# Performance work log

Hardware: AMD Instinct MI355X
Metric: run time of the kernel (lower is better)

## Reference

```python
import jax, jax.numpy as jnp
import numpy as np

NEG = -1e20
EPS = float(np.finfo(np.float32).eps)


def setup_inputs() -> dict:
    key = jax.random.key(0)
    k1, k2, k3, k4 = jax.random.split(key, 4)
    B, S, E, D = 8, 2048, 1024, 1024
    return {
        "embeddings": jax.random.normal(k1, (B, S, E), dtype=jnp.float32),
        "mask": jnp.ones((B, S), dtype=jnp.int32),
        "W_q": jax.random.normal(k2, (E, D), dtype=jnp.float32),
        "W_k": jax.random.normal(k3, (E, D), dtype=jnp.float32),
        "W_v": jax.random.normal(k4, (E, D), dtype=jnp.float32),
    }


def reference(embeddings, mask, W_q, W_k, W_v):
    # embeddings: [B,S,E]; mask: [B,S] (1 = keep, 0 = pad)
    q = embeddings @ W_q            # [B,S,D]
    k = embeddings @ W_k            # [B,S,D]
    v = embeddings @ W_v            # [B,S,Dv]
    energy = jnp.einsum("bqd,bkd->bqk", q, k)  # [B,S,S]
    S = embeddings.shape[1]
    causal = jnp.tril(jnp.ones((S, S), dtype=bool))          # [S,S]
    energy = jnp.where(causal[None, :, :], energy, NEG)
    pad = (mask == 0)[:, None, :]                             # [B,1,S]
    energy = jnp.where(pad, NEG, energy)
    d_k = jnp.float32(W_k.shape[1])
    scale = jnp.sqrt(d_k) + EPS
    attention = jax.nn.softmax(energy / scale, axis=-1)       # [B,S,S]
    output = jnp.einsum("bqk,bkd->bqd", attention, v)         # [B,S,Dv]
    return output, attention
```

## Files before the change

kernel.cpp:

```cpp
#include <hip/hip_runtime.h>

#define Bb 8
#define Ss 2048
#define Ee 1024
#define Dd 1024

typedef __attribute__((ext_vector_type(8))) __bf16 bf16x8;
typedef __attribute__((ext_vector_type(4))) float f32x4;
typedef unsigned short u16;

__device__ __forceinline__ u16 f2bf(float x) {
  unsigned u = __float_as_uint(x);
  return (u16)((u + 0x7fffu + ((u >> 16) & 1u)) >> 16);
}
__device__ __forceinline__ float bf2f(u16 h) {
  return __uint_as_float(((unsigned)h) << 16);
}

__device__ __forceinline__ void gload16(const void* g, void* l) {
  __builtin_amdgcn_global_load_lds(
      (__attribute__((address_space(1))) void*)const_cast<void*>(g),
      (__attribute__((address_space(3))) void*)l, 16, 0, 0);
}

#define MFMA_BF16 __builtin_amdgcn_mfma_f32_16x16x32_bf16

__global__ __launch_bounds__(256) void k_split4(const float* __restrict__ in,
                                                u16* __restrict__ hi,
                                                u16* __restrict__ lo,
                                                long long n4) {
  long long i = (long long)blockIdx.x * 256 + threadIdx.x;
  if (i >= n4) return;
  float4 v = ((const float4*)in)[i];
  float xs[4] = {v.x, v.y, v.z, v.w};
  u16 hh[4], ll[4];
#pragma unroll
  for (int j = 0; j < 4; ++j) {
    hh[j] = f2bf(xs[j]);
    ll[j] = f2bf(xs[j] - bf2f(hh[j]));
  }
  ushort4 h, l;
  h.x = hh[0]; h.y = hh[1]; h.z = hh[2]; h.w = hh[3];
  l.x = ll[0]; l.y = ll[1]; l.z = ll[2]; l.w = ll[3];
  ((ushort4*)hi)[i] = h;
  ((ushort4*)lo)[i] = l;
}

__global__ __launch_bounds__(256) void k_wt_split(const float* __restrict__ W,
                                                  u16* __restrict__ hi,
                                                  u16* __restrict__ lo) {
  __shared__ float t[32][33];
  const int tx = threadIdx.x & 31;
  const int ty = threadIdx.x >> 5;
  const int e0 = blockIdx.y * 32, d0 = blockIdx.x * 32;
#pragma unroll
  for (int r = ty; r < 32; r += 8)
    t[r][tx] = W[(long long)(e0 + r) * Dd + d0 + tx];
  __syncthreads();
#pragma unroll
  for (int r = ty; r < 32; r += 8) {
    float x = t[tx][r];
    long long o = (long long)(d0 + r) * Ee + e0 + tx;
    u16 h = f2bf(x);
    hi[o] = h;
    if (lo) lo[o] = f2bf(x - bf2f(h));
  }
}

template <int NP, int EPI, bool CAUSAL, bool TRIK>
__global__ __launch_bounds__(512, 4) void k_t128(
    const u16* __restrict__ Ah, const u16* __restrict__ Al,
    const u16* __restrict__ Bh, const u16* __restrict__ Bl,
    float* __restrict__ Cf, u16* __restrict__ Ch, u16* __restrict__ Cl,
    int nbx, int N, int K, long long strA, long long strB, long long strC) {
  constexpr int NMAT = (NP == 3) ? 4 : 2;
  const int nwg = gridDim.x;
  const int f = blockIdx.x;
  const int wgid = (f & 7) * (nwg >> 3) + (f >> 3);
  int bx, by, bz;
  if (CAUSAL) {
    bz = wgid / 136;
    const int t = wgid % 136;
    int yy = 0, c = 0;
    while (c + yy + 1 <= t) { c += yy + 1; ++yy; }
    by = yy;
    bx = t - c;
  } else {
    bz = blockIdx.y;
    bx = wgid % nbx;
    by = wgid / nbx;
  }

  __shared__ __align__(16) u16 lds[2][NMAT][4096];

  const int tid = threadIdx.x;
  const int lane = tid & 63;
  const int w = tid >> 6;
  const int wr = w >> 1;
  const int wc = w & 1;

  const u16* srcBase[NMAT];
  if constexpr (NP == 3) {
    srcBase[0] = Ah + (long long)bz * strA;
    srcBase[1] = Al + (long long)bz * strA;
    srcBase[2] = Bh + (long long)bz * strB;
    srcBase[3] = Bl + (long long)bz * strB;
  } else {
    srcBase[0] = Ah + (long long)bz * strA;
    srcBase[1] = Bh + (long long)bz * strB;
  }
  const long long row0[2] = {(long long)by * 128, (long long)bx * 128};

  const int rL = tid >> 2;
  const int colOff = ((tid & 3) ^ ((tid >> 3) & 3)) * 8;
  const int rdOff = (lane & 15) * 64 + ((((lane >> 4) & 3) ^ ((lane >> 1) & 3)) << 4);

  const int AR = wr * 32;
  const int BR = wc * 64;
  int nt = K / 32;
  if (TRIK) {
    const int lim = ((by + 1) * 128) / 32;
    if (lim < nt) nt = lim;
  }

  const u16* gp[NMAT];
#pragma unroll
  for (int m = 0; m < NMAT; ++m) {
    const int opsel = (NP == 3) ? (m >> 1) : m;
    gp[m] = srcBase[m] + (row0[opsel] + rL) * (long long)K + colOff;
  }

#define STG(BUF)                                                       \
  {                                                                    \
    _Pragma("unroll") for (int m = 0; m < NMAT; ++m) {                 \
      gload16(gp[m], (char*)&lds[BUF][m][0] + tid * 16);               \
      gp[m] += 32;                                                     \
    }                                                                  \
  }
#define LDFRAG(MAT, R) \
  (*(const bf16x8*)((const char*)&lds[cur][MAT][0] + (R)*64 + rdOff))
#define BAR __builtin_amdgcn_s_barrier()

#define CLUSTER3(NH)                                                         \
  __builtin_amdgcn_s_setprio(1);                                             \
  _Pragma("unroll") for (int m = 0; m < 2; ++m)                              \
      _Pragma("unroll") for (int n = 0; n < 2; ++n)                          \
          acc[m][(NH)*2 + n] =                                               \
      MFMA_BF16(aH[m], bL[n], acc[m][(NH)*2 + n], 0, 0, 0);                  \
  _Pragma("unroll") for (int m = 0; m < 2; ++m)                              \
      _Pragma("unroll") for (int n = 0; n < 2; ++n)                          \
          acc[m][(NH)*2 + n] =                                               \
      MFMA_BF16(aL[m], bH[n], acc[m][(NH)*2 + n], 0, 0, 0);                  \
  _Pragma("unroll") for (int m = 0; m < 2; ++m)                              \
      _Pragma("unroll") for (int n = 0; n < 2; ++n)                          \
          acc[m][(NH)*2 + n] =                                               \
      MFMA_BF16(aH[m], bH[n], acc[m][(NH)*2 + n], 0, 0, 0);                  \
  __builtin_amdgcn_s_setprio(0);

  f32x4 acc[2][4];
#pragma unroll
  for (int m = 0; m < 2; ++m)
#pragma unroll
    for (int n = 0; n < 4; ++n) acc[m][n] = f32x4{0.f, 0.f, 0.f, 0.f};

  bf16x8 aH[2], aL[2], bH[2], bL[2];
  bf16x8 bF[4];

  STG(0);

  for (int kt = 0; kt < nt; ++kt) {
    const int cur = kt & 1;
    const bool more = (kt + 1 < nt);

    if (more) {
      STG(cur ^ 1);
      if constexpr (NP == 3)
        asm volatile("s_waitcnt vmcnt(4)" ::: "memory");
      else
        asm volatile("s_waitcnt vmcnt(2)" ::: "memory");
    } else {
      asm volatile("s_waitcnt vmcnt(0)" ::: "memory");
    }
    BAR;

    if constexpr (NP == 3) {
#pragma unroll
      for (int m = 0; m < 2; ++m) {
        aH[m] = LDFRAG(0, AR + m * 16);
        aL[m] = LDFRAG(1, AR + m * 16);
      }
#pragma unroll
      for (int n = 0; n < 2; ++n) {
        bH[n] = LDFRAG(2, BR + n * 16);
        bL[n] = LDFRAG(3, BR + n * 16);
      }
      BAR;
      CLUSTER3(0);
      BAR;
#pragma unroll
      for (int n = 0; n < 2; ++n) {
        bH[n] = LDFRAG(2, BR + 32 + n * 16);
        bL[n] = LDFRAG(3, BR + 32 + n * 16);
      }
      BAR;
      CLUSTER3(1);
      BAR;
    } else {
#pragma unroll
      for (int m = 0; m < 2; ++m) aH[m] = LDFRAG(0, AR + m * 16);
#pragma unroll
      for (int n = 0; n < 4; ++n) bF[n] = LDFRAG(1, BR + n * 16);
      BAR;
      __builtin_amdgcn_s_setprio(1);
#pragma unroll
      for (int m = 0; m < 2; ++m)
#pragma unroll
        for (int n = 0; n < 4; ++n)
          acc[m][n] = MFMA_BF16(aH[m], bF[n], acc[m][n], 0, 0, 0);
      __builtin_amdgcn_s_setprio(0);
      BAR;
    }
  }

  const int cr = (lane >> 4) << 2;
  const int cc = lane & 15;
#pragma unroll
  for (int m = 0; m < 2; ++m)
#pragma unroll
    for (int n = 0; n < 4; ++n)
#pragma unroll
      for (int r = 0; r < 4; ++r) {
        const long long row = (long long)by * 128 + wr * 32 + m * 16 + cr + r;
        const long long col = (long long)bx * 128 + wc * 64 + n * 16 + cc;
        const float v = acc[m][n][r];
        if constexpr (EPI == 0) {
          Cf[(long long)bz * strC + row * N + col] = v;
        } else if constexpr (EPI == 1) {
          const long long idx = row * N + col;
          u16 h = f2bf(v);
          Ch[idx] = h;
          Cl[idx] = f2bf(v - bf2f(h));
        } else {
          Ch[(long long)bz * strC + row * N + col] = f2bf(v);
        }
      }
#undef STG
#undef LDFRAG
#undef BAR
#undef CLUSTER3
}

__global__ __launch_bounds__(256) void k_softmax(float* __restrict__ attn,
                                                 u16* __restrict__ attn_bf,
                                                 const int* __restrict__ mask,
                                                 float inv_scale) {
  const int q = blockIdx.x;
  const int b = blockIdx.y;
  const int tid = threadIdx.x;
  float* row = attn + ((long long)b * Ss + q) * Ss;
  u16* rowb = attn_bf + ((long long)b * Ss + q) * Ss;
  const int* mrow = mask + b * Ss;
  const int qup = ((q >> 7) + 1) << 7;

  float x[8];
  float m = -3.0e38f;
#pragma unroll
  for (int j = 0; j < 8; ++j) {
    const int k = tid + j * 256;
    float v = -3.0e38f;
    if (k <= q) {
      const float e = row[k];
      v = ((mrow[k] != 0) ? e : -1e20f) * inv_scale;
    }
    x[j] = v;
    m = fmaxf(m, v);
  }
#pragma unroll
  for (int o = 32; o > 0; o >>= 1) m = fmaxf(m, __shfl_xor(m, o));
  __shared__ float redm[4], reds[4];
  const int w = tid >> 6;
  if ((tid & 63) == 0) redm[w] = m;
  __syncthreads();
  m = fmaxf(fmaxf(redm[0], redm[1]), fmaxf(redm[2], redm[3]));
  float s = 0.f;
#pragma unroll
  for (int j = 0; j < 8; ++j) {
    x[j] = __expf(x[j] - m);
    s += x[j];
  }
#pragma unroll
  for (int o = 32; o > 0; o >>= 1) s += __shfl_xor(s, o);
  if ((tid & 63) == 0) reds[w] = s;
  __syncthreads();
  s = reds[0] + reds[1] + reds[2] + reds[3];
  const float inv = 1.0f / s;
#pragma unroll
  for (int j = 0; j < 8; ++j) {
    const int k = tid + j * 256;
    if (k <= q) {
      const float a = x[j] * inv;
      row[k] = a;
      rowb[k] = f2bf(a);
    } else {
      row[k] = 0.0f;
      if (k < qup) rowb[k] = 0;
    }
  }
}

extern "C" void kernel_launch(void* const* d_in, const int* in_sizes, int n_in,
                              void* d_out, int out_size, void* d_ws, size_t ws_size,
                              hipStream_t stream) {
  const float* emb = (const float*)d_in[0];
  const int* mask = (const int*)d_in[1];
  const float* Wq = (const float*)d_in[2];
  const float* Wk = (const float*)d_in[3];
  const float* Wv = (const float*)d_in[4];

  float* out = (float*)d_out;
  float* attn = out + (long long)Bb * Ss * Dd;

  char* p = (char*)d_ws;
  u16* emb_hi = (u16*)p;
  u16* emb_lo = emb_hi + 16777216LL;
  u16* R_hi = (u16*)(p + 67108864LL);
  u16* R_lo = R_hi + 16777216LL;
  u16* v_t = R_lo + 16777216LL;
  u16* attn_bf = v_t + 16777216LL;
  u16* Wqr_hi = attn_bf + 16777216LL;
  u16* Wqr_lo = Wqr_hi + 1048576LL;
  u16* Wkr_hi = Wqr_lo + 1048576LL;
  u16* Wkr_lo = Wkr_hi + 1048576LL;
  u16* M_hi = Wkr_lo + 1048576LL;
  u16* M_lo = M_hi + 1048576LL;
  u16* WvT_hi = M_lo + 1048576LL;

  const float inv_scale = 1.0f / (32.0f + 1.1920929e-07f);

  k_split4<<<16384, 256, 0, stream>>>(emb, emb_hi, emb_lo, 4194304LL);
  k_split4<<<1024, 256, 0, stream>>>(Wq, Wqr_hi, Wqr_lo, 262144LL);
  k_split4<<<1024, 256, 0, stream>>>(Wk, Wkr_hi, Wkr_lo, 262144LL);
  k_wt_split<<<dim3(32, 32), 256, 0, stream>>>(Wv, WvT_hi, nullptr);

  k_t128<3, 1, false, false><<<64, 512, 0, stream>>>(
      Wkr_hi, Wkr_lo, Wqr_hi, Wqr_lo, nullptr, M_hi, M_lo,
      8, 1024, 1024, 0, 0, 0);
  k_t128<3, 1, false, false><<<1024, 512, 0, stream>>>(
      emb_hi, emb_lo, M_hi, M_lo, nullptr, R_hi, R_lo,
      8, 1024, 1024, 0, 0, 0);
  k_t128<1, 2, false, false><<<dim3(128, 8), 512, 0, stream>>>(
      WvT_hi, nullptr, emb_hi, nullptr, nullptr, v_t, nullptr,
      16, Ss, Ee, 0, (long long)Ss * Ee, (long long)Dd * Ss);
  k_t128<3, 0, true, false><<<1088, 512, 0, stream>>>(
      R_hi, R_lo, emb_hi, emb_lo, attn, nullptr, nullptr,
      0, Ss, Dd, (long long)Ss * Dd, (long long)Ss * Dd, (long long)Ss * Ss);
  k_softmax<<<dim3(Ss, Bb), 256, 0, stream>>>(attn, attn_bf, mask, inv_scale);
  k_t128<1, 0, false, true><<<dim3(128, 8), 512, 0, stream>>>(
      attn_bf, nullptr, v_t, nullptr, out, nullptr, nullptr,
      8, Dd, Ss, (long long)Ss * Ss, (long long)Dd * Ss, (long long)Ss * Dd);
}
```

Baseline: 469.6 us.

## Enlarge GEMM tiles to 256x128 with 64x64 per-warp output blocks

Changes the shared GEMM kernel from 128x128 to 256x128 workgroup tiles, so each warp now computes a 64x64 block (4x4 MFMA fragments) instead of 32x64. This raises operand reuse from LDS and drops the extra mid-iteration barriers and split fragment loads. The causal tile enumeration, the softmax padding boundary and all grid sizes are updated to match. In exchange it uses more LDS and registers per workgroup (min occupancy lowered to 2 for the 3-pass path) and launches fewer workgroups, which may hurt load balance.

```diff
diff --git a/kernel.cpp b/kernel.cpp
--- a/kernel.cpp
+++ b/kernel.cpp
@@ -68,21 +68,27 @@
 }
 
 template <int NP, int EPI, bool CAUSAL, bool TRIK>
-__global__ __launch_bounds__(512, 4) void k_t128(
+__global__ __launch_bounds__(512, (NP == 3) ? 2 : 4) void k_t256(
     const u16* __restrict__ Ah, const u16* __restrict__ Al,
     const u16* __restrict__ Bh, const u16* __restrict__ Bl,
     float* __restrict__ Cf, u16* __restrict__ Ch, u16* __restrict__ Cl,
     int nbx, int N, int K, long long strA, long long strB, long long strC) {
-  constexpr int NMAT = (NP == 3) ? 4 : 2;
+  constexpr int NLD = (NP == 3) ? 6 : 3;
+  constexpr int LDSB = (NP == 3) ? 49152 : 24576;
+  constexpr int OFF_AL = 16384;
+  constexpr int OFF_BH = (NP == 3) ? 32768 : 16384;
+  constexpr int OFF_BL = 40960;
+  __shared__ __align__(16) char lds[2][LDSB];
+
   const int nwg = gridDim.x;
   const int f = blockIdx.x;
   const int wgid = (f & 7) * (nwg >> 3) + (f >> 3);
   int bx, by, bz;
   if (CAUSAL) {
-    bz = wgid / 136;
-    const int t = wgid % 136;
+    bz = wgid / 72;
+    const int t = wgid % 72;
     int yy = 0, c = 0;
-    while (c + yy + 1 <= t) { c += yy + 1; ++yy; }
+    while (c + 2 * yy + 2 <= t) { c += 2 * yy + 2; ++yy; }
     by = yy;
     bx = t - c;
   } else {
@@ -91,80 +97,62 @@
     by = wgid / nbx;
   }
 
-  __shared__ __align__(16) u16 lds[2][NMAT][4096];
-
   const int tid = threadIdx.x;
   const int lane = tid & 63;
   const int w = tid >> 6;
   const int wr = w >> 1;
   const int wc = w & 1;
-
-  const u16* srcBase[NMAT];
-  if constexpr (NP == 3) {
-    srcBase[0] = Ah + (long long)bz * strA;
-    srcBase[1] = Al + (long long)bz * strA;
-    srcBase[2] = Bh + (long long)bz * strB;
-    srcBase[3] = Bl + (long long)bz * strB;
-  } else {
-    srcBase[0] = Ah + (long long)bz * strA;
-    srcBase[1] = Bh + (long long)bz * strB;
-  }
-  const long long row0[2] = {(long long)by * 128, (long long)bx * 128};
+  const int AR = wr * 64;
+  const int BR = wc * 64;
 
   const int rL = tid >> 2;
   const int colOff = ((tid & 3) ^ ((tid >> 3) & 3)) * 8;
   const int rdOff = (lane & 15) * 64 + ((((lane >> 4) & 3) ^ ((lane >> 1) & 3)) << 4);
 
-  const int AR = wr * 32;
-  const int BR = wc * 64;
+  const long long rowA0 = (long long)by * 256;
+  const long long rowB0 = (long long)bx * 128;
+
   int nt = K / 32;
   if (TRIK) {
-    const int lim = ((by + 1) * 128) / 32;
+    const int lim = (by + 1) * 8;
     if (lim < nt) nt = lim;
   }
 
-  const u16* gp[NMAT];
-#pragma unroll
-  for (int m = 0; m < NMAT; ++m) {
-    const int opsel = (NP == 3) ? (m >> 1) : m;
-    gp[m] = srcBase[m] + (row0[opsel] + rL) * (long long)K + colOff;
-  }
-
-#define STG(BUF)                                                       \
-  {                                                                    \
-    _Pragma("unroll") for (int m = 0; m < NMAT; ++m) {                 \
-      gload16(gp[m], (char*)&lds[BUF][m][0] + tid * 16);               \
-      gp[m] += 32;                                                     \
-    }                                                                  \
-  }
-#define LDFRAG(MAT, R) \
-  (*(const bf16x8*)((const char*)&lds[cur][MAT][0] + (R)*64 + rdOff))
+  const u16* gp[NLD];
+  int dst[NLD];
+  if constexpr (NP == 3) {
+    const u16* pAh = Ah + (long long)bz * strA;
+    const u16* pAl = Al + (long long)bz * strA;
+    const u16* pBh = Bh + (long long)bz * strB;
+    const u16* pBl = Bl + (long long)bz * strB;
+    gp[0] = pAh + (rowA0 + rL) * (long long)K + colOff;       dst[0] = tid * 16;
+    gp[1] = pAh + (rowA0 + 128 + rL) * (long long)K + colOff; dst[1] = 8192 + tid * 16;
+    gp[2] = pAl + (rowA0 + rL) * (long long)K + colOff;       dst[2] = OFF_AL + tid * 16;
+    gp[3] = pAl + (rowA0 + 128 + rL) * (long long)K + colOff; dst[3] = OFF_AL + 8192 + tid * 16;
+    gp[4] = pBh + (rowB0 + rL) * (long long)K + colOff;       dst[4] = OFF_BH + tid * 16;
+    gp[5] = pBl + (rowB0 + rL) * (long long)K + colOff;       dst[5] = OFF_BL + tid * 16;
+  } else {
+    const u16* pA = Ah + (long long)bz * strA;
+    const u16* pB = Bh + (long long)bz * strB;
+    gp[0] = pA + (rowA0 + rL) * (long long)K + colOff;        dst[0] = tid * 16;
+    gp[1] = pA + (rowA0 + 128 + rL) * (long long)K + colOff;  dst[1] = 8192 + tid * 16;
+    gp[2] = pB + (rowB0 + rL) * (long long)K + colOff;        dst[2] = OFF_BH + tid * 16;
+  }
+
+#define STG(BUF)                                               \
+  {                                                            \
+    _Pragma("unroll") for (int u = 0; u < NLD; ++u) {          \
+      gload16(gp[u], lds[BUF] + dst[u]);                       \
+      gp[u] += 32;                                             \
+    }                                                          \
+  }
 #define BAR __builtin_amdgcn_s_barrier()
 
-#define CLUSTER3(NH)                                                         \
-  __builtin_amdgcn_s_setprio(1);                                             \
-  _Pragma("unroll") for (int m = 0; m < 2; ++m)                              \
-      _Pragma("unroll") for (int n = 0; n < 2; ++n)                          \
-          acc[m][(NH)*2 + n] =                                               \
-      MFMA_BF16(aH[m], bL[n], acc[m][(NH)*2 + n], 0, 0, 0);                  \
-  _Pragma("unroll") for (int m = 0; m < 2; ++m)                              \
-      _Pragma("unroll") for (int n = 0; n < 2; ++n)                          \
-          acc[m][(NH)*2 + n] =                                               \
-      MFMA_BF16(aL[m], bH[n], acc[m][(NH)*2 + n], 0, 0, 0);                  \
-  _Pragma("unroll") for (int m = 0; m < 2; ++m)                              \
-      _Pragma("unroll") for (int n = 0; n < 2; ++n)                          \
-          acc[m][(NH)*2 + n] =                                               \
-      MFMA_BF16(aH[m], bH[n], acc[m][(NH)*2 + n], 0, 0, 0);                  \
-  __builtin_amdgcn_s_setprio(0);
-
-  f32x4 acc[2][4];
-#pragma unroll
-  for (int m = 0; m < 2; ++m)
+  f32x4 acc[4][4];
+#pragma unroll
+  for (int m = 0; m < 4; ++m)
 #pragma unroll
     for (int n = 0; n < 4; ++n) acc[m][n] = f32x4{0.f, 0.f, 0.f, 0.f};
-
-  bf16x8 aH[2], aL[2], bH[2], bL[2];
-  bf16x8 bF[4];
 
   STG(0);
 
@@ -175,63 +163,69 @@
     if (more) {
       STG(cur ^ 1);
       if constexpr (NP == 3)
-        asm volatile("s_waitcnt vmcnt(4)" ::: "memory");
+        asm volatile("s_waitcnt vmcnt(6)" ::: "memory");
       else
-        asm volatile("s_waitcnt vmcnt(2)" ::: "memory");
+        asm volatile("s_waitcnt vmcnt(3)" ::: "memory");
     } else {
       asm volatile("s_waitcnt vmcnt(0)" ::: "memory");
     }
     BAR;
 
+    const char* bb = lds[cur];
     if constexpr (NP == 3) {
-#pragma unroll
-      for (int m = 0; m < 2; ++m) {
-        aH[m] = LDFRAG(0, AR + m * 16);
-        aL[m] = LDFRAG(1, AR + m * 16);
+      bf16x8 aH[4], aL[4], bH[4], bL[4];
+#pragma unroll
+      for (int m = 0; m < 4; ++m) {
+        aH[m] = *(const bf16x8*)(bb + (AR + m * 16) * 64 + rdOff);
+        aL[m] = *(const bf16x8*)(bb + OFF_AL + (AR + m * 16) * 64 + rdOff);
       }
 #pragma unroll
-      for (int n = 0; n < 2; ++n) {
-        bH[n] = LDFRAG(2, BR + n * 16);
-        bL[n] = LDFRAG(3, BR + n * 16);
+      for (int n = 0; n < 4; ++n) {
+        bH[n] = *(const bf16x8*)(bb + OFF_BH + (BR + n * 16) * 64 + rdOff);
+        bL[n] = *(const bf16x8*)(bb + OFF_BL + (BR + n * 16) * 64 + rdOff);
       }
-      BAR;
-      CLUSTER3(0);
-      BAR;
-#pragma unroll
-      for (int n = 0; n < 2; ++n) {
-        bH[n] = LDFRAG(2, BR + 32 + n * 16);
-        bL[n] = LDFRAG(3, BR + 32 + n * 16);
-      }
-      BAR;
-      CLUSTER3(1);
-      BAR;
+#pragma unroll
+      for (int m = 0; m < 4; ++m)
+#pragma unroll
+        for (int n = 0; n < 4; ++n)
+          acc[m][n] = MFMA_BF16(aH[m], bL[n], acc[m][n], 0, 0, 0);
+#pragma unroll
+      for (int m = 0; m < 4; ++m)
+#pragma unroll
+        for (int n = 0; n < 4; ++n)
+          acc[m][n] = MFMA_BF16(aL[m], bH[n], acc[m][n], 0, 0, 0);
+#pragma unroll
+      for (int m = 0; m < 4; ++m)
+#pragma unroll
+        for (int n = 0; n < 4; ++n)
+          acc[m][n] = MFMA_BF16(aH[m], bH[n], acc[m][n], 0, 0, 0);
     } else {
-#pragma unroll
-      for (int m = 0; m < 2; ++m) aH[m] = LDFRAG(0, AR + m * 16);
-#pragma unroll
-      for (int n = 0; n < 4; ++n) bF[n] = LDFRAG(1, BR + n * 16);
-      BAR;
-      __builtin_amdgcn_s_setprio(1);
-#pragma unroll
-      for (int m = 0; m < 2; ++m)
+      bf16x8 a[4], b[4];
+#pragma unroll
+      for (int m = 0; m < 4; ++m)
+        a[m] = *(const bf16x8*)(bb + (AR + m * 16) * 64 + rdOff);
+#pragma unroll
+      for (int n = 0; n < 4; ++n)
+        b[n] = *(const bf16x8*)(bb + OFF_BH + (BR + n * 16) * 64 + rdOff);
+#pragma unroll
+      for (int m = 0; m < 4; ++m)
 #pragma unroll
         for (int n = 0; n < 4; ++n)
-          acc[m][n] = MFMA_BF16(aH[m], bF[n], acc[m][n], 0, 0, 0);
-      __builtin_amdgcn_s_setprio(0);
-      BAR;
+          acc[m][n] = MFMA_BF16(a[m], b[n], acc[m][n], 0, 0, 0);
     }
+    BAR;
   }
 
   const int cr = (lane >> 4) << 2;
   const int cc = lane & 15;
 #pragma unroll
-  for (int m = 0; m < 2; ++m)
+  for (int m = 0; m < 4; ++m)
 #pragma unroll
     for (int n = 0; n < 4; ++n)
 #pragma unroll
       for (int r = 0; r < 4; ++r) {
-        const long long row = (long long)by * 128 + wr * 32 + m * 16 + cr + r;
-        const long long col = (long long)bx * 128 + wc * 64 + n * 16 + cc;
+        const long long row = (long long)by * 256 + AR + m * 16 + cr + r;
+        const long long col = (long long)bx * 128 + BR + n * 16 + cc;
         const float v = acc[m][n][r];
         if constexpr (EPI == 0) {
           Cf[(long long)bz * strC + row * N + col] = v;
@@ -245,9 +239,7 @@
         }
       }
 #undef STG
-#undef LDFRAG
 #undef BAR
-#undef CLUSTER3
 }
 
 __global__ __launch_bounds__(256) void k_softmax(float* __restrict__ attn,
@@ -260,7 +252,7 @@
   float* row = attn + ((long long)b * Ss + q) * Ss;
   u16* rowb = attn_bf + ((long long)b * Ss + q) * Ss;
   const int* mrow = mask + b * Ss;
-  const int qup = ((q >> 7) + 1) << 7;
+  const int qup = ((q >> 8) + 1) << 8;
 
   float x[8];
   float m = -3.0e38f;
@@ -342,20 +334,20 @@
   k_split4<<<1024, 256, 0, stream>>>(Wk, Wkr_hi, Wkr_lo, 262144LL);
   k_wt_split<<<dim3(32, 32), 256, 0, stream>>>(Wv, WvT_hi, nullptr);
 
-  k_t128<3, 1, false, false><<<64, 512, 0, stream>>>(
+  k_t256<3, 1, false, false><<<32, 512, 0, stream>>>(
       Wkr_hi, Wkr_lo, Wqr_hi, Wqr_lo, nullptr, M_hi, M_lo,
       8, 1024, 1024, 0, 0, 0);
-  k_t128<3, 1, false, false><<<1024, 512, 0, stream>>>(
+  k_t256<3, 1, false, false><<<512, 512, 0, stream>>>(
       emb_hi, emb_lo, M_hi, M_lo, nullptr, R_hi, R_lo,
       8, 1024, 1024, 0, 0, 0);
-  k_t128<1, 2, false, false><<<dim3(128, 8), 512, 0, stream>>>(
+  k_t256<1, 2, false, false><<<dim3(64, 8), 512, 0, stream>>>(
       WvT_hi, nullptr, emb_hi, nullptr, nullptr, v_t, nullptr,
       16, Ss, Ee, 0, (long long)Ss * Ee, (long long)Dd * Ss);
-  k_t128<3, 0, true, false><<<1088, 512, 0, stream>>>(
+  k_t256<3, 0, true, false><<<576, 512, 0, stream>>>(
       R_hi, R_lo, emb_hi, emb_lo, attn, nullptr, nullptr,
-      0, Ss, Dd, (long long)Ss * Dd, (long long)Ss * Dd, (long long)Ss * Ss);
+      0, Ss, Dd, (long long)Ss * Dd, (long long)Ss * Ee, (long long)Ss * Ss);
   k_softmax<<<dim3(Ss, Bb), 256, 0, stream>>>(attn, attn_bf, mask, inv_scale);
-  k_t128<1, 0, false, true><<<dim3(128, 8), 512, 0, stream>>>(
+  k_t256<1, 0, false, true><<<dim3(64, 8), 512, 0, stream>>>(
       attn_bf, nullptr, v_t, nullptr, out, nullptr, nullptr,
       8, Dd, Ss, (long long)Ss * Ss, (long long)Dd * Ss, (long long)Ss * Dd);
 }
```

Measured after the change: 468.7 us. Within noise of the previous version (-0.2%).

## Use 256x128 output tiles for projection, V and attention-times-V GEMMs

Applied to the files above, without the earlier changes.

Adds two new GEMM kernels with 256-row by 128-column tiles: a split-precision kernel (hi/lo bf16, three MFMA passes) for the emb·M projection, and a double-buffered single-precision-bf16 kernel for the V projection and the attention·V product. The larger tiles are meant to raise reuse of each B tile and halve the number of workgroups. The softmax zero-fill boundary is widened from 128 to 256 to match the triangular K limit of the new P·V tile. The split kernel has no double buffering, so load latency may be exposed, and the bigger tiles reduce parallelism for the smaller grids.

```diff
diff --git a/kernel.cpp b/kernel.cpp
--- a/kernel.cpp
+++ b/kernel.cpp
@@ -250,6 +250,218 @@
 #undef CLUSTER3
 }
 
+template <int EPI>
+__global__ __launch_bounds__(512, 4) void k_s256(
+    const u16* __restrict__ Ah, const u16* __restrict__ Al,
+    const u16* __restrict__ Bh, const u16* __restrict__ Bl,
+    float* __restrict__ Cf, u16* __restrict__ Ch, u16* __restrict__ Cl,
+    int nbx, int N, int K) {
+  constexpr int OFF_AL = 16384;
+  constexpr int OFF_BH = 32768;
+  constexpr int OFF_BL = 40960;
+  __shared__ __align__(16) char lds[49152];
+
+  const int nwg = gridDim.x;
+  const int f = blockIdx.x;
+  const int wgid = (f & 7) * (nwg >> 3) + (f >> 3);
+  const int bx = wgid % nbx;
+  const int by = wgid / nbx;
+
+  const int tid = threadIdx.x;
+  const int lane = tid & 63;
+  const int w = tid >> 6;
+  const int wr = w >> 1;
+  const int wc = w & 1;
+  const int AR = wr * 64;
+  const int BR = wc * 64;
+
+  const int rL = tid >> 2;
+  const int colOff = ((tid & 3) ^ ((tid >> 3) & 3)) * 8;
+  const int rdOff = (lane & 15) * 64 + ((((lane >> 4) & 3) ^ ((lane >> 1) & 3)) << 4);
+
+  const long long rowA0 = (long long)by * 256;
+  const long long rowB0 = (long long)bx * 128;
+  const int nt = K / 32;
+
+  const u16* gp[6];
+  int dst[6];
+  gp[0] = Ah + (rowA0 + rL) * (long long)K + colOff;        dst[0] = tid * 16;
+  gp[1] = Ah + (rowA0 + 128 + rL) * (long long)K + colOff;  dst[1] = 8192 + tid * 16;
+  gp[2] = Al + (rowA0 + rL) * (long long)K + colOff;        dst[2] = OFF_AL + tid * 16;
+  gp[3] = Al + (rowA0 + 128 + rL) * (long long)K + colOff;  dst[3] = OFF_AL + 8192 + tid * 16;
+  gp[4] = Bh + (rowB0 + rL) * (long long)K + colOff;        dst[4] = OFF_BH + tid * 16;
+  gp[5] = Bl + (rowB0 + rL) * (long long)K + colOff;        dst[5] = OFF_BL + tid * 16;
+
+  f32x4 acc[4][4];
+#pragma unroll
+  for (int m = 0; m < 4; ++m)
+#pragma unroll
+    for (int n = 0; n < 4; ++n) acc[m][n] = f32x4{0.f, 0.f, 0.f, 0.f};
+
+  for (int kt = 0; kt < nt; ++kt) {
+#pragma unroll
+    for (int u = 0; u < 6; ++u) {
+      gload16(gp[u], lds + dst[u]);
+      gp[u] += 32;
+    }
+    asm volatile("s_waitcnt vmcnt(0)" ::: "memory");
+    __builtin_amdgcn_s_barrier();
+
+    bf16x8 aH[4], aL[4];
+#pragma unroll
+    for (int m = 0; m < 4; ++m) {
+      aH[m] = *(const bf16x8*)(lds + (AR + m * 16) * 64 + rdOff);
+      aL[m] = *(const bf16x8*)(lds + OFF_AL + (AR + m * 16) * 64 + rdOff);
+    }
+#pragma unroll
+    for (int n = 0; n < 4; ++n) {
+      bf16x8 bH = *(const bf16x8*)(lds + OFF_BH + (BR + n * 16) * 64 + rdOff);
+      bf16x8 bL = *(const bf16x8*)(lds + OFF_BL + (BR + n * 16) * 64 + rdOff);
+#pragma unroll
+      for (int m = 0; m < 4; ++m)
+        acc[m][n] = MFMA_BF16(aH[m], bL, acc[m][n], 0, 0, 0);
+#pragma unroll
+      for (int m = 0; m < 4; ++m)
+        acc[m][n] = MFMA_BF16(aL[m], bH, acc[m][n], 0, 0, 0);
+#pragma unroll
+      for (int m = 0; m < 4; ++m)
+        acc[m][n] = MFMA_BF16(aH[m], bH, acc[m][n], 0, 0, 0);
+    }
+    __builtin_amdgcn_s_barrier();
+  }
+
+  const int cr = (lane >> 4) << 2;
+  const int cc = lane & 15;
+#pragma unroll
+  for (int m = 0; m < 4; ++m)
+#pragma unroll
+    for (int n = 0; n < 4; ++n)
+#pragma unroll
+      for (int r = 0; r < 4; ++r) {
+        const long long row = (long long)by * 256 + AR + m * 16 + cr + r;
+        const long long col = (long long)bx * 128 + BR + n * 16 + cc;
+        const float v = acc[m][n][r];
+        if constexpr (EPI == 0) {
+          Cf[row * N + col] = v;
+        } else {
+          const long long idx = row * N + col;
+          u16 h = f2bf(v);
+          Ch[idx] = h;
+          Cl[idx] = f2bf(v - bf2f(h));
+        }
+      }
+}
+
+template <int EPI, bool TRIK>
+__global__ __launch_bounds__(512, 4) void k_t256(
+    const u16* __restrict__ Ah, const u16* __restrict__ Bh,
+    float* __restrict__ Cf, u16* __restrict__ Ch,
+    int nbx, int N, int K, long long strA, long long strB, long long strC) {
+  constexpr int OFF_BH = 16384;
+  __shared__ __align__(16) char lds[2][24576];
+
+  const int nwg = gridDim.x;
+  const int f = blockIdx.x;
+  const int wgid = (f & 7) * (nwg >> 3) + (f >> 3);
+  const int bz = blockIdx.y;
+  const int bx = wgid % nbx;
+  const int by = wgid / nbx;
+
+  const int tid = threadIdx.x;
+  const int lane = tid & 63;
+  const int w = tid >> 6;
+  const int wr = w >> 1;
+  const int wc = w & 1;
+  const int AR = wr * 64;
+  const int BR = wc * 64;
+
+  const int rL = tid >> 2;
+  const int colOff = ((tid & 3) ^ ((tid >> 3) & 3)) * 8;
+  const int rdOff = (lane & 15) * 64 + ((((lane >> 4) & 3) ^ ((lane >> 1) & 3)) << 4);
+
+  const long long rowA0 = (long long)by * 256;
+  const long long rowB0 = (long long)bx * 128;
+
+  int nt = K / 32;
+  if (TRIK) {
+    const int lim = (by + 1) * 8;
+    if (lim < nt) nt = lim;
+  }
+
+  const u16* pA = Ah + (long long)bz * strA;
+  const u16* pB = Bh + (long long)bz * strB;
+  const u16* gp[3];
+  int dst[3];
+  gp[0] = pA + (rowA0 + rL) * (long long)K + colOff;        dst[0] = tid * 16;
+  gp[1] = pA + (rowA0 + 128 + rL) * (long long)K + colOff;  dst[1] = 8192 + tid * 16;
+  gp[2] = pB + (rowB0 + rL) * (long long)K + colOff;        dst[2] = OFF_BH + tid * 16;
+
+#define STG(BUF)                                               \
+  {                                                            \
+    _Pragma("unroll") for (int u = 0; u < 3; ++u) {            \
+      gload16(gp[u], lds[BUF] + dst[u]);                       \
+      gp[u] += 32;                                             \
+    }                                                          \
+  }
+#define BAR __builtin_amdgcn_s_barrier()
+
+  f32x4 acc[4][4];
+#pragma unroll
+  for (int m = 0; m < 4; ++m)
+#pragma unroll
+    for (int n = 0; n < 4; ++n) acc[m][n] = f32x4{0.f, 0.f, 0.f, 0.f};
+
+  STG(0);
+
+  for (int kt = 0; kt < nt; ++kt) {
+    const int cur = kt & 1;
+    const bool more = (kt + 1 < nt);
+
+    if (more) {
+      STG(cur ^ 1);
+      asm volatile("s_waitcnt vmcnt(3)" ::: "memory");
+    } else {
+      asm volatile("s_waitcnt vmcnt(0)" ::: "memory");
+    }
+    BAR;
+
+    const char* bb = lds[cur];
+    bf16x8 a[4], b[4];
+#pragma unroll
+    for (int m = 0; m < 4; ++m)
+      a[m] = *(const bf16x8*)(bb + (AR + m * 16) * 64 + rdOff);
+#pragma unroll
+    for (int n = 0; n < 4; ++n)
+      b[n] = *(const bf16x8*)(bb + OFF_BH + (BR + n * 16) * 64 + rdOff);
+#pragma unroll
+    for (int m = 0; m < 4; ++m)
+#pragma unroll
+      for (int n = 0; n < 4; ++n)
+        acc[m][n] = MFMA_BF16(a[m], b[n], acc[m][n], 0, 0, 0);
+    BAR;
+  }
+
+  const int cr = (lane >> 4) << 2;
+  const int cc = lane & 15;
+#pragma unroll
+  for (int m = 0; m < 4; ++m)
+#pragma unroll
+    for (int n = 0; n < 4; ++n)
+#pragma unroll
+      for (int r = 0; r < 4; ++r) {
+        const long long row = (long long)by * 256 + AR + m * 16 + cr + r;
+        const long long col = (long long)bx * 128 + BR + n * 16 + cc;
+        const float v = acc[m][n][r];
+        if constexpr (EPI == 0) {
+          Cf[(long long)bz * strC + row * N + col] = v;
+        } else {
+          Ch[(long long)bz * strC + row * N + col] = f2bf(v);
+        }
+      }
+#undef STG
+#undef BAR
+}
+
 __global__ __launch_bounds__(256) void k_softmax(float* __restrict__ attn,
                                                  u16* __restrict__ attn_bf,
                                                  const int* __restrict__ mask,
@@ -260,7 +472,7 @@
   float* row = attn + ((long long)b * Ss + q) * Ss;
   u16* rowb = attn_bf + ((long long)b * Ss + q) * Ss;
   const int* mrow = mask + b * Ss;
-  const int qup = ((q >> 7) + 1) << 7;
+  const int qup = ((q >> 8) + 1) << 8;
 
   float x[8];
   float m = -3.0e38f;
@@ -345,17 +557,16 @@
   k_t128<3, 1, false, false><<<64, 512, 0, stream>>>(
       Wkr_hi, Wkr_lo, Wqr_hi, Wqr_lo, nullptr, M_hi, M_lo,
       8, 1024, 1024, 0, 0, 0);
-  k_t128<3, 1, false, false><<<1024, 512, 0, stream>>>(
-      emb_hi, emb_lo, M_hi, M_lo, nullptr, R_hi, R_lo,
-      8, 1024, 1024, 0, 0, 0);
-  k_t128<1, 2, false, false><<<dim3(128, 8), 512, 0, stream>>>(
-      WvT_hi, nullptr, emb_hi, nullptr, nullptr, v_t, nullptr,
+  k_s256<1><<<512, 512, 0, stream>>>(
+      emb_hi, emb_lo, M_hi, M_lo, nullptr, R_hi, R_lo, 8, 1024, 1024);
+  k_t256<2, false><<<dim3(64, 8), 512, 0, stream>>>(
+      WvT_hi, emb_hi, nullptr, v_t,
       16, Ss, Ee, 0, (long long)Ss * Ee, (long long)Dd * Ss);
   k_t128<3, 0, true, false><<<1088, 512, 0, stream>>>(
       R_hi, R_lo, emb_hi, emb_lo, attn, nullptr, nullptr,
       0, Ss, Dd, (long long)Ss * Dd, (long long)Ss * Dd, (long long)Ss * Ss);
   k_softmax<<<dim3(Ss, Bb), 256, 0, stream>>>(attn, attn_bf, mask, inv_scale);
-  k_t128<1, 0, false, true><<<dim3(128, 8), 512, 0, stream>>>(
-      attn_bf, nullptr, v_t, nullptr, out, nullptr, nullptr,
+  k_t256<0, true><<<dim3(64, 8), 512, 0, stream>>>(
+      attn_bf, v_t, out, nullptr,
       8, Dd, Ss, (long long)Ss * Ss, (long long)Dd * Ss, (long long)Ss * Dd);
 }
```

Measured after the change: 449.6 us. 1.04x faster.
